# Performance work log

Hardware: AMD Instinct MI355X
Metric: run time of the kernel (lower is better)

The kernel has to match this reference:

```python
import jax, jax.numpy as jnp
import numpy as np

N_NODES = 50000
N_EDGES = 800000
D_IN = 128
D_HID = 128
GN_EPS = 1e-5
L2_EPS = 1e-12


def _gcn_conv(x, edge_index, W, b, num_nodes):
    """PyG GCNConv: symmetric normalization with self-loops; x [N, Fin]."""
    src, dst = edge_index[0], edge_index[1]
    loops = jnp.arange(num_nodes, dtype=src.dtype)
    src = jnp.concatenate([src, loops])
    dst = jnp.concatenate([dst, loops])
    ew = jnp.ones(src.shape[0], dtype=x.dtype)
    deg = jax.ops.segment_sum(ew, dst, num_segments=num_nodes)
    dinv = jnp.where(deg > 0, jax.lax.rsqrt(deg), 0.0)
    norm = dinv[src] * dinv[dst]                       # [E+N]
    xw = x @ W                                         # [N, Fout]
    msg = xw[src] * norm[:, None]                      # gather + scale
    out = jax.ops.segment_sum(msg, dst, num_segments=num_nodes)
    return out + b


def _message_norm(x, msg, scale):
    """PyG MessageNorm(learn_scale=True): x + scale * ||x|| * msg/||msg||."""
    msg_n = msg / jnp.maximum(jnp.linalg.norm(msg, axis=-1, keepdims=True), L2_EPS)
    x_norm = jnp.linalg.norm(x, axis=-1, keepdims=True)
    return x + scale * x_norm * msg_n


def _graph_norm(x, weight, bias, mean_scale):
    """PyG GraphNorm, single graph (batch all zeros)."""
    mean = jnp.mean(x, axis=0, keepdims=True)
    out = x - mean * mean_scale
    var = jnp.mean(out * out, axis=0, keepdims=True)
    return weight * out * jax.lax.rsqrt(var + GN_EPS) + bias


def _gelu(x):
    return jax.nn.gelu(x, approximate=False)


def setup_inputs() -> dict:
    key = jax.random.key(0)
    ks = jax.random.split(key, 4)
    X = jax.random.normal(ks[0], (D_IN, N_NODES), dtype=jnp.float32)
    edge_index = jax.random.randint(ks[1], (2, N_EDGES), 0, N_NODES, dtype=jnp.int64)
    W1 = jax.random.normal(ks[2], (D_IN, D_HID), dtype=jnp.float32) * (1.0 / np.sqrt(D_IN))
    b1 = jnp.zeros((D_HID,), dtype=jnp.float32)
    scale1 = jnp.ones((1,), dtype=jnp.float32)
    W2 = jax.random.normal(ks[3], (D_HID, D_IN), dtype=jnp.float32) * (1.0 / np.sqrt(D_HID))
    b2 = jnp.zeros((D_IN,), dtype=jnp.float32)
    scale2 = jnp.ones((1,), dtype=jnp.float32)
    gn_weight = jnp.ones((D_IN,), dtype=jnp.float32)
    gn_bias = jnp.zeros((D_IN,), dtype=jnp.float32)
    gn_mean_scale = jnp.ones((D_IN,), dtype=jnp.float32)
    return {"X": X, "edge_index": edge_index, "W1": W1, "b1": b1, "scale1": scale1,
            "W2": W2, "b2": b2, "scale2": scale2, "gn_weight": gn_weight,
            "gn_bias": gn_bias, "gn_mean_scale": gn_mean_scale}


def reference(X, edge_index, W1, b1, scale1, W2, b2, scale2,
              gn_weight, gn_bias, gn_mean_scale):
    x = X.T                                            # [N, D_IN]
    n = x.shape[0]
    # GCNChain 1
    f = _gelu(_message_norm(x, _gcn_conv(x, edge_index, W1, b1, n), scale1))
    # GCNChain 2
    f = _gelu(_message_norm(f, _gcn_conv(f, edge_index, W2, b2, n), scale2))
    # residual + GraphNorm + GELU
    return _gelu(_graph_norm(f + x, gn_weight, gn_bias, gn_mean_scale))
```

## Files before the change

### kernel.cpp

```cpp
#include <hip/hip_runtime.h>
#include <math.h>

#define D 128
#define CAP 64
#define NBUCK 98
#define BSZ   512
#define CAPB  10240

typedef _Float16 h8 __attribute__((ext_vector_type(8)));
typedef float f4x __attribute__((ext_vector_type(4)));

__device__ __forceinline__ float gelu_f(float v){
    return 0.5f * v * (1.0f + erff(v * 0.70710678f));
}

__global__ void k_init(float* colsum, float* colsq, int* gcur,
                       const float* __restrict__ W1, const float* __restrict__ W2,
                       _Float16* __restrict__ wz1, _Float16* __restrict__ wz2){
    int i = blockIdx.x*blockDim.x + threadIdx.x;
    if (i < D){ colsum[i] = 0.f; colsq[i] = 0.f; }
    if (i < NBUCK) gcur[i] = 0;
    if (i < 32768){
        const float* W = (i < 16384) ? W1 : W2;
        _Float16* wz   = (i < 16384) ? wz1 : wz2;
        int u = i & 16383;
        int jj = u & 7, l = (u>>3)&63, fi = u>>9;
        int kb = fi>>3, j = fi&7;
        int k = kb*32 + (l>>4)*8 + jj;
        int c = j*16 + (l&15);
        wz[u] = (_Float16)W[k*D + c];
    }
}

__global__ __launch_bounds__(256)
void k_part(const int* __restrict__ ei, int* __restrict__ gcur,
            unsigned int* __restrict__ ebin, int E){
    __shared__ int bcnt[NBUCK], bbase[NBUCK], bcur[NBUCK];
    int t = threadIdx.x;
    int chunk = (E + gridDim.x - 1) / gridDim.x;
    int e0 = blockIdx.x*chunk, e1 = min(e0 + chunk, E);
    if (t < NBUCK){ bcnt[t] = 0; bcur[t] = 0; }
    __syncthreads();
    int sl[13], dl[13];
    #pragma unroll
    for (int k = 0; k < 13; k++){
        int e = e0 + t + k*256;
        sl[k] = -1;
        if (e < e1){
            sl[k] = __builtin_nontemporal_load(&ei[e]);
            dl[k] = __builtin_nontemporal_load(&ei[E + e]);
            atomicAdd(&bcnt[dl[k] >> 9], 1);
        }
    }
    __syncthreads();
    if (t < NBUCK) bbase[t] = atomicAdd(&gcur[t], bcnt[t]);
    __syncthreads();
    #pragma unroll
    for (int k = 0; k < 13; k++){
        if (sl[k] >= 0){
            int d = dl[k], b = d >> 9;
            int p = atomicAdd(&bcur[b], 1);
            int idx = bbase[b] + p;
            if (idx < CAPB)
                ebin[(size_t)b*CAPB + idx] = ((unsigned)(d & (BSZ-1)) << 16) | (unsigned)sl[k];
        }
    }
}

__global__ __launch_bounds__(256)
void k_fill2(const unsigned int* __restrict__ ebin, const int* __restrict__ gcur,
             int* __restrict__ cnt, unsigned short* __restrict__ csrc, int N){
    __shared__ unsigned short slab[BSZ*CAP];
    __shared__ int lcnt[BSZ];
    int b = blockIdx.x, t = threadIdx.x;
    for (int i = t; i < BSZ; i += 256) lcnt[i] = 0;
    __syncthreads();
    int cntb = gcur[b]; if (cntb > CAPB) cntb = CAPB;
    const unsigned int* bp = ebin + (size_t)b*CAPB;
    for (int e = t; e < cntb; e += 256){
        unsigned pk = __builtin_nontemporal_load(&bp[e]);
        int dl = pk >> 16;
        int p = atomicAdd(&lcnt[dl], 1);
        if (p < CAP) slab[dl*CAP + p] = (unsigned short)(pk & 0xFFFF);
    }
    __syncthreads();
    int base = b*BSZ;
    int nvalid = N - base; if (nvalid > BSZ) nvalid = BSZ; if (nvalid < 0) nvalid = 0;
    uint4* dst = (uint4*)&csrc[(size_t)base*CAP];
    const uint4* src = (const uint4*)slab;
    for (int i = t; i < nvalid*8; i += 256) dst[i] = src[i];
    for (int i = t; i < nvalid; i += 256) cnt[base + i] = lcnt[i];
}

__launch_bounds__(256)
__global__ void k_gemm_mfma(const float* __restrict__ in, const h8* __restrict__ wz,
                            const int* __restrict__ cnt, _Float16* __restrict__ outh,
                            h8* __restrict__ xt16, int N){
    __shared__ _Float16 a_lds[8192];
    int t = threadIdx.x;
    int n0 = blockIdx.x * 64;

    #pragma unroll
    for (int i = 0; i < 32; i++){
        int idx = i*256 + t;
        int k = idx >> 6, nn = idx & 63;
        int n = n0 + nn;
        float v = (n < N) ? in[(size_t)k*N + n] : 0.f;
        int kb = k>>5, ks = k&31;
        int lane = (ks>>3)*16 + (nn&15);
        int w = nn>>4;
        a_lds[((kb*4 + w)*64 + lane)*8 + (ks&7)] = (_Float16)v;
    }
    __syncthreads();

    int w = t>>6, l = t&63;
    f4x acc[8];
    #pragma unroll
    for (int j = 0; j < 8; j++) acc[j] = (f4x){0.f, 0.f, 0.f, 0.f};
    #pragma unroll
    for (int kb = 0; kb < 4; kb++){
        h8 a = *(const h8*)&a_lds[((kb*4 + w)*64 + l)*8];
        #pragma unroll
        for (int j = 0; j < 8; j++){
            h8 b = wz[(kb*8 + j)*64 + l];
            acc[j] = __builtin_amdgcn_mfma_f32_16x16x32_f16(a, b, acc[j], 0, 0, 0);
        }
    }

    int quad = l>>4, m = l&15;
    #pragma unroll
    for (int r = 0; r < 4; r++){
        int node = n0 + w*16 + quad*4 + r;
        if (node < N){
            float dv = rsqrtf((float)(cnt[node] + 1));
            #pragma unroll
            for (int j = 0; j < 8; j++)
                outh[(size_t)node*D + j*16 + m] = (_Float16)(acc[j][r] * dv);
        }
    }

    {
        int node = t>>2, kb = t&3;
        int n = n0 + node;
        if (n < N){
            #pragma unroll
            for (int q = 0; q < 4; q++){
                h8 v = *(const h8*)&a_lds[((kb*4 + (node>>4))*64 + q*16 + (node&15))*8];
                xt16[(size_t)n*16 + kb*4 + q] = v;
            }
        }
    }
}

__launch_bounds__(256)
__global__ void k_gath1(const h8* __restrict__ y, const h8* __restrict__ resid,
                        const int* __restrict__ cnt,
                        const unsigned short* __restrict__ csrc,
                        const float* __restrict__ bias, const float* __restrict__ scale,
                        const h8* __restrict__ wz,
                        h8* __restrict__ f1out, _Float16* __restrict__ y2out, int N){
    __shared__ _Float16 a_lds[8192];
    int t = threadIdx.x;
    int n0 = blockIdx.x * 64;
    int g = t >> 4, lane = t & 15;
    int kb = lane >> 2, q = lane & 3;
    const float4* bp = (const float4*)&bias[lane*8];
    float4 b0 = bp[0], b1v = bp[1];
    float sc0 = scale[0];

    for (int it = 0; it < 4; it++){
        int n = n0 + it*16 + g;
        bool valid = (n < N);
        h8 a0 = {0,0,0,0,0,0,0,0}, a1 = a0, a2 = a0, a3 = a0;
        int m = 0; float dv = 1.f;
        if (valid){
            int mraw = cnt[n];
            dv = rsqrtf((float)(mraw + 1));
            m = (mraw < CAP) ? mraw : CAP;
            a0 = y[(size_t)n*16 + lane];
        }
        const unsigned short* sp = csrc + (size_t)n*CAP;
        int j = 0;
        for (; j + 8 <= m; j += 8){
            int s0 = sp[j+0], s1 = sp[j+1], s2 = sp[j+2], s3 = sp[j+3];
            int s4 = sp[j+4], s5 = sp[j+5], s6 = sp[j+6], s7 = sp[j+7];
            h8 v0 = y[(size_t)s0*16 + lane];
            h8 v1 = y[(size_t)s1*16 + lane];
            h8 v2 = y[(size_t)s2*16 + lane];
            h8 v3 = y[(size_t)s3*16 + lane];
            h8 v4 = y[(size_t)s4*16 + lane];
            h8 v5 = y[(size_t)s5*16 + lane];
            h8 v6 = y[(size_t)s6*16 + lane];
            h8 v7 = y[(size_t)s7*16 + lane];
            a0 += v0; a1 += v1; a2 += v2; a3 += v3;
            a0 += v4; a1 += v5; a2 += v6; a3 += v7;
        }
        for (; j + 4 <= m; j += 4){
            int s0 = sp[j+0], s1 = sp[j+1], s2 = sp[j+2], s3 = sp[j+3];
            h8 v0 = y[(size_t)s0*16 + lane];
            h8 v1 = y[(size_t)s1*16 + lane];
            h8 v2 = y[(size_t)s2*16 + lane];
            h8 v3 = y[(size_t)s3*16 + lane];
            a0 += v0; a1 += v1; a2 += v2; a3 += v3;
        }
        for (; j < m; j++) a1 += y[(size_t)sp[j]*16 + lane];
        h8 ah = (a0 + a1) + (a2 + a3);

        float c[8], r[8];
        float nc = 0.f, nr = 0.f;
        h8 rv = {0,0,0,0,0,0,0,0};
        if (valid) rv = resid[(size_t)n*16 + lane];
        #pragma unroll
        for (int i = 0; i < 8; i++){
            float bb = (i < 4) ? (&b0.x)[i] : (&b1v.x)[i-4];
            c[i] = bb + dv * (float)ah[i];
            nc += c[i]*c[i];
            r[i] = (float)rv[i];
            nr += r[i]*r[i];
        }
        #pragma unroll
        for (int mm = 8; mm > 0; mm >>= 1){
            nc += __shfl_xor(nc, mm, 64);
            nr += __shfl_xor(nr, mm, 64);
        }
        float scl = sc0 * sqrtf(nr) / fmaxf(sqrtf(nc), 1e-12f);
        h8 o;
        #pragma unroll
        for (int i = 0; i < 8; i++) o[i] = (_Float16)gelu_f(r[i] + scl*c[i]);
        if (valid) f1out[(size_t)n*16 + lane] = o;
        *(h8*)&a_lds[((kb*4 + it)*64 + q*16 + g)*8] = o;
    }
    __syncthreads();

    int w = t>>6, l = t&63;
    f4x acc[8];
    #pragma unroll
    for (int j = 0; j < 8; j++) acc[j] = (f4x){0.f, 0.f, 0.f, 0.f};
    #pragma unroll
    for (int kb2 = 0; kb2 < 4; kb2++){
        h8 a = *(const h8*)&a_lds[((kb2*4 + w)*64 + l)*8];
        #pragma unroll
        for (int j = 0; j < 8; j++){
            h8 b = wz[(kb2*8 + j)*64 + l];
            acc[j] = __builtin_amdgcn_mfma_f32_16x16x32_f16(a, b, acc[j], 0, 0, 0);
        }
    }
    int quad = l>>4, mcol = l&15;
    #pragma unroll
    for (int r2 = 0; r2 < 4; r2++){
        int node = n0 + w*16 + quad*4 + r2;
        if (node < N){
            float dv = rsqrtf((float)(cnt[node] + 1));
            #pragma unroll
            for (int j = 0; j < 8; j++)
                y2out[(size_t)node*D + j*16 + mcol] = (_Float16)(acc[j][r2] * dv);
        }
    }
}

__launch_bounds__(256)
__global__ void k_gather2(const h8* __restrict__ y, const h8* __restrict__ resid,
                          const h8* __restrict__ xorig,
                          const int* __restrict__ cnt,
                          const unsigned short* __restrict__ csrc,
                          const float* __restrict__ bias, const float* __restrict__ scale,
                          h8* __restrict__ out16, int N){
    int n = blockIdx.x*16 + (threadIdx.x >> 4);
    if (n >= N) return;
    int lane = threadIdx.x & 15;
    h8 a0 = y[(size_t)n*16 + lane];
    h8 a1 = {0,0,0,0,0,0,0,0}, a2 = a1, a3 = a1;
    int mraw = cnt[n];
    float dv = rsqrtf((float)(mraw + 1));
    int m = (mraw < CAP) ? mraw : CAP;
    const unsigned short* sp = csrc + (size_t)n*CAP;
    int j = 0;
    for (; j + 8 <= m; j += 8){
        int s0 = sp[j+0], s1 = sp[j+1], s2 = sp[j+2], s3 = sp[j+3];
        int s4 = sp[j+4], s5 = sp[j+5], s6 = sp[j+6], s7 = sp[j+7];
        h8 v0 = y[(size_t)s0*16 + lane];
        h8 v1 = y[(size_t)s1*16 + lane];
        h8 v2 = y[(size_t)s2*16 + lane];
        h8 v3 = y[(size_t)s3*16 + lane];
        h8 v4 = y[(size_t)s4*16 + lane];
        h8 v5 = y[(size_t)s5*16 + lane];
        h8 v6 = y[(size_t)s6*16 + lane];
        h8 v7 = y[(size_t)s7*16 + lane];
        a0 += v0; a1 += v1; a2 += v2; a3 += v3;
        a0 += v4; a1 += v5; a2 += v6; a3 += v7;
    }
    for (; j + 4 <= m; j += 4){
        int s0 = sp[j+0], s1 = sp[j+1], s2 = sp[j+2], s3 = sp[j+3];
        h8 v0 = y[(size_t)s0*16 + lane];
        h8 v1 = y[(size_t)s1*16 + lane];
        h8 v2 = y[(size_t)s2*16 + lane];
        h8 v3 = y[(size_t)s3*16 + lane];
        a0 += v0; a1 += v1; a2 += v2; a3 += v3;
    }
    for (; j < m; j++) a1 += y[(size_t)sp[j]*16 + lane];
    h8 ah = (a0 + a1) + (a2 + a3);

    const float4* bp = (const float4*)&bias[lane*8];
    float4 b0 = bp[0], b1v = bp[1];
    float c[8], r[8];
    float nc = 0.f, nr = 0.f;
    h8 rv = resid[(size_t)n*16 + lane];
    #pragma unroll
    for (int i = 0; i < 8; i++){
        float bb = (i < 4) ? (&b0.x)[i] : (&b1v.x)[i-4];
        c[i] = bb + dv * (float)ah[i];
        nc += c[i]*c[i];
        r[i] = (float)rv[i];
        nr += r[i]*r[i];
    }
    #pragma unroll
    for (int mm = 8; mm > 0; mm >>= 1){
        nc += __shfl_xor(nc, mm, 64);
        nr += __shfl_xor(nr, mm, 64);
    }
    float scl = scale[0] * sqrtf(nr) / fmaxf(sqrtf(nc), 1e-12f);
    h8 xv = xorig[(size_t)n*16 + lane];
    h8 o;
    #pragma unroll
    for (int i = 0; i < 8; i++)
        o[i] = (_Float16)(gelu_f(r[i] + scl*c[i]) + (float)xv[i]);
    out16[(size_t)n*16 + lane] = o;
}

__global__ void k_stats(const _Float16* __restrict__ h, float* colsum, float* colsq, int N){
    __shared__ float ls[256], ls2[256];
    int t = threadIdx.x;
    int f = t & 127, half = t >> 7;
    float s = 0.f, s2 = 0.f;
    for (int n = blockIdx.x*2 + half; n < N; n += gridDim.x*2){
        float v = (float)h[(size_t)n*D + f]; s += v; s2 += v*v;
    }
    ls[t] = s; ls2[t] = s2;
    __syncthreads();
    if (t < 128){
        s  = ls[t]  + ls[t+128];
        s2 = ls2[t] + ls2[t+128];
        atomicAdd(&colsum[f], s);
        atomicAdd(&colsq[f], s2);
    }
}

__global__ void k_final(const h8* __restrict__ h16,
                        const float* __restrict__ colsum, const float* __restrict__ colsq,
                        const float* __restrict__ gw, const float* __restrict__ gb,
                        const float* __restrict__ ms,
                        float* __restrict__ outp, int N){
    __shared__ float cf[D], sh[D];
    int t = threadIdx.x;
    if (t < D){
        float invN = 1.0f / (float)N;
        float mean = colsum[t] * invN;
        float c = mean * ms[t];
        float var = colsq[t]*invN - 2.f*c*mean + c*c;
        float a = gw[t] * rsqrtf(var + 1e-5f);
        cf[t] = a;
        sh[t] = gb[t] - c*a;
    }
    __syncthreads();
    int i = blockIdx.x*blockDim.x + t;
    if (i < N*16){
        int n = i >> 4, lane = i & 15;
        h8 v = h16[i];
        int f = lane*8;
        float4 o0, o1;
        o0.x = gelu_f((float)v[0]*cf[f+0] + sh[f+0]);
        o0.y = gelu_f((float)v[1]*cf[f+1] + sh[f+1]);
        o0.z = gelu_f((float)v[2]*cf[f+2] + sh[f+2]);
        o0.w = gelu_f((float)v[3]*cf[f+3] + sh[f+3]);
        o1.x = gelu_f((float)v[4]*cf[f+4] + sh[f+4]);
        o1.y = gelu_f((float)v[5]*cf[f+5] + sh[f+5]);
        o1.z = gelu_f((float)v[6]*cf[f+6] + sh[f+6]);
        o1.w = gelu_f((float)v[7]*cf[f+7] + sh[f+7]);
        *(float4*)&outp[(size_t)n*D + f]     = o0;
        *(float4*)&outp[(size_t)n*D + f + 4] = o1;
    }
}

extern "C" void kernel_launch(void* const* d_in, const int* in_sizes, int n_in,
                              void* d_out, int out_size, void* d_ws, size_t ws_size,
                              hipStream_t stream){
    const float* X   = (const float*)d_in[0];
    const int*   ei  = (const int*)  d_in[1];
    const float* W1  = (const float*)d_in[2];
    const float* b1  = (const float*)d_in[3];
    const float* s1  = (const float*)d_in[4];
    const float* W2  = (const float*)d_in[5];
    const float* b2  = (const float*)d_in[6];
    const float* s2  = (const float*)d_in[7];
    const float* gw  = (const float*)d_in[8];
    const float* gb  = (const float*)d_in[9];
    const float* gms = (const float*)d_in[10];
    int N = in_sizes[0] / D;
    int E = in_sizes[1] / 2;
    float* out = (float*)d_out;

    char* ws = (char*)d_ws;
    size_t o = 0;
    auto alloc = [&](size_t bytes)->void*{
        o = (o + 255) & ~(size_t)255;
        void* p = ws + o; o += bytes; return p;
    };
    int*            cnt    = (int*)           alloc((size_t)N * sizeof(int));
    unsigned short* csrc   = (unsigned short*)alloc((size_t)N * CAP * sizeof(unsigned short));
    unsigned int*   ebin   = (unsigned int*)  alloc((size_t)NBUCK * CAPB * sizeof(unsigned int));
    int*            gcur   = (int*)           alloc(NBUCK * sizeof(int));
    float*          colsum = (float*)         alloc(D * sizeof(float));
    float*          colsq  = (float*)         alloc(D * sizeof(float));
    _Float16*       wz1    = (_Float16*)      alloc(16384 * sizeof(_Float16));
    _Float16*       wz2    = (_Float16*)      alloc(16384 * sizeof(_Float16));
    _Float16*       A      = (_Float16*)      alloc((size_t)N * D * sizeof(_Float16));
    _Float16*       A2     = (_Float16*)      alloc((size_t)N * D * sizeof(_Float16));
    h8*             XT16   = (h8*)            alloc((size_t)N * D * sizeof(_Float16));
    h8*             F1     = (h8*)            alloc((size_t)N * D * sizeof(_Float16));
    h8*             B16    = (h8*)            alloc((size_t)N * D * sizeof(_Float16));

    k_init<<<128, 256, 0, stream>>>(colsum, colsq, gcur, W1, W2, wz1, wz2);
    k_part<<<256, 256, 0, stream>>>(ei, gcur, ebin, E);
    k_fill2<<<NBUCK, 256, 0, stream>>>(ebin, gcur, cnt, csrc, N);

    k_gemm_mfma<<<(N+63)/64, 256, 0, stream>>>(X, (const h8*)wz1, cnt, A, XT16, N);
    k_gath1<<<(N+63)/64, 256, 0, stream>>>((const h8*)A, XT16, cnt, csrc, b1, s1,
                                           (const h8*)wz2, F1, A2, N);
    k_gather2<<<(N+15)/16, 256, 0, stream>>>((const h8*)A2, F1, XT16,
                                             cnt, csrc, b2, s2, B16, N);
    k_stats<<<256, 256, 0, stream>>>((const _Float16*)B16, colsum, colsq, N);
    k_final<<<(N*16+255)/256, 256, 0, stream>>>(B16, colsum, colsq, gw, gb, gms, out, N);
}
```

Before: 263.9 us.

## Shrink gather1 blocks to 16 nodes and split MFMA output columns across warps

The first gather+GEMM kernel now handles 16 nodes per block instead of 64, so there is no serial 4-iteration gather loop and the grid has four times as many blocks. This gives more parallelism and latency hiding for the random neighbour gathers. The fused second-layer GEMM is re-split so each of the four waves computes two 16-column output tiles for the same 16 nodes, using a padded LDS layout that avoids bank conflicts. The cost is that each block reloads the weight matrix for only 16 nodes, so weight traffic per node rises fourfold.

```diff
diff --git a/kernel.cpp b/kernel.cpp
--- a/kernel.cpp
+++ b/kernel.cpp
@@ -159,101 +159,95 @@
                         const float* __restrict__ bias, const float* __restrict__ scale,
                         const h8* __restrict__ wz,
                         h8* __restrict__ f1out, _Float16* __restrict__ y2out, int N){
-    __shared__ _Float16 a_lds[8192];
+    __shared__ _Float16 a_lds[16*17*8];
     int t = threadIdx.x;
-    int n0 = blockIdx.x * 64;
+    int n0 = blockIdx.x * 16;
     int g = t >> 4, lane = t & 15;
-    int kb = lane >> 2, q = lane & 3;
+    int n = n0 + g;
+    bool valid = (n < N);
+
+    h8 a0 = {0,0,0,0,0,0,0,0}, a1 = a0, a2 = a0, a3 = a0;
+    int m = 0; float dv = 1.f;
+    if (valid){
+        int mraw = cnt[n];
+        dv = rsqrtf((float)(mraw + 1));
+        m = (mraw < CAP) ? mraw : CAP;
+        a0 = y[(size_t)n*16 + lane];
+    }
+    const unsigned short* sp = csrc + (size_t)n*CAP;
+    int j = 0;
+    for (; j + 8 <= m; j += 8){
+        int s0 = sp[j+0], s1 = sp[j+1], s2 = sp[j+2], s3 = sp[j+3];
+        int s4 = sp[j+4], s5 = sp[j+5], s6 = sp[j+6], s7 = sp[j+7];
+        h8 v0 = y[(size_t)s0*16 + lane];
+        h8 v1 = y[(size_t)s1*16 + lane];
+        h8 v2 = y[(size_t)s2*16 + lane];
+        h8 v3 = y[(size_t)s3*16 + lane];
+        h8 v4 = y[(size_t)s4*16 + lane];
+        h8 v5 = y[(size_t)s5*16 + lane];
+        h8 v6 = y[(size_t)s6*16 + lane];
+        h8 v7 = y[(size_t)s7*16 + lane];
+        a0 += v0; a1 += v1; a2 += v2; a3 += v3;
+        a0 += v4; a1 += v5; a2 += v6; a3 += v7;
+    }
+    for (; j + 4 <= m; j += 4){
+        int s0 = sp[j+0], s1 = sp[j+1], s2 = sp[j+2], s3 = sp[j+3];
+        h8 v0 = y[(size_t)s0*16 + lane];
+        h8 v1 = y[(size_t)s1*16 + lane];
+        h8 v2 = y[(size_t)s2*16 + lane];
+        h8 v3 = y[(size_t)s3*16 + lane];
+        a0 += v0; a1 += v1; a2 += v2; a3 += v3;
+    }
+    for (; j < m; j++) a1 += y[(size_t)sp[j]*16 + lane];
+    h8 ah = (a0 + a1) + (a2 + a3);
+
     const float4* bp = (const float4*)&bias[lane*8];
     float4 b0 = bp[0], b1v = bp[1];
-    float sc0 = scale[0];
-
-    for (int it = 0; it < 4; it++){
-        int n = n0 + it*16 + g;
-        bool valid = (n < N);
-        h8 a0 = {0,0,0,0,0,0,0,0}, a1 = a0, a2 = a0, a3 = a0;
-        int m = 0; float dv = 1.f;
-        if (valid){
-            int mraw = cnt[n];
-            dv = rsqrtf((float)(mraw + 1));
-            m = (mraw < CAP) ? mraw : CAP;
-            a0 = y[(size_t)n*16 + lane];
-        }
-        const unsigned short* sp = csrc + (size_t)n*CAP;
-        int j = 0;
-        for (; j + 8 <= m; j += 8){
-            int s0 = sp[j+0], s1 = sp[j+1], s2 = sp[j+2], s3 = sp[j+3];
-            int s4 = sp[j+4], s5 = sp[j+5], s6 = sp[j+6], s7 = sp[j+7];
-            h8 v0 = y[(size_t)s0*16 + lane];
-            h8 v1 = y[(size_t)s1*16 + lane];
-            h8 v2 = y[(size_t)s2*16 + lane];
-            h8 v3 = y[(size_t)s3*16 + lane];
-            h8 v4 = y[(size_t)s4*16 + lane];
-            h8 v5 = y[(size_t)s5*16 + lane];
-            h8 v6 = y[(size_t)s6*16 + lane];
-            h8 v7 = y[(size_t)s7*16 + lane];
-            a0 += v0; a1 += v1; a2 += v2; a3 += v3;
-            a0 += v4; a1 += v5; a2 += v6; a3 += v7;
-        }
-        for (; j + 4 <= m; j += 4){
-            int s0 = sp[j+0], s1 = sp[j+1], s2 = sp[j+2], s3 = sp[j+3];
-            h8 v0 = y[(size_t)s0*16 + lane];
-            h8 v1 = y[(size_t)s1*16 + lane];
-            h8 v2 = y[(size_t)s2*16 + lane];
-            h8 v3 = y[(size_t)s3*16 + lane];
-            a0 += v0; a1 += v1; a2 += v2; a3 += v3;
-        }
-        for (; j < m; j++) a1 += y[(size_t)sp[j]*16 + lane];
-        h8 ah = (a0 + a1) + (a2 + a3);
-
-        float c[8], r[8];
-        float nc = 0.f, nr = 0.f;
-        h8 rv = {0,0,0,0,0,0,0,0};
-        if (valid) rv = resid[(size_t)n*16 + lane];
-        #pragma unroll
-        for (int i = 0; i < 8; i++){
-            float bb = (i < 4) ? (&b0.x)[i] : (&b1v.x)[i-4];
-            c[i] = bb + dv * (float)ah[i];
-            nc += c[i]*c[i];
-            r[i] = (float)rv[i];
-            nr += r[i]*r[i];
-        }
-        #pragma unroll
-        for (int mm = 8; mm > 0; mm >>= 1){
-            nc += __shfl_xor(nc, mm, 64);
-            nr += __shfl_xor(nr, mm, 64);
-        }
-        float scl = sc0 * sqrtf(nr) / fmaxf(sqrtf(nc), 1e-12f);
-        h8 o;
+    float c[8], r[8];
+    float nc = 0.f, nr = 0.f;
+    h8 rv = {0,0,0,0,0,0,0,0};
+    if (valid) rv = resid[(size_t)n*16 + lane];
+    #pragma unroll
+    for (int i = 0; i < 8; i++){
+        float bb = (i < 4) ? (&b0.x)[i] : (&b1v.x)[i-4];
+        c[i] = bb + dv * (float)ah[i];
+        nc += c[i]*c[i];
+        r[i] = (float)rv[i];
+        nr += r[i]*r[i];
+    }
+    #pragma unroll
+    for (int mm = 8; mm > 0; mm >>= 1){
+        nc += __shfl_xor(nc, mm, 64);
+        nr += __shfl_xor(nr, mm, 64);
+    }
+    float scl = scale[0] * sqrtf(nr) / fmaxf(sqrtf(nc), 1e-12f);
+    h8 o = {0,0,0,0,0,0,0,0};
+    if (valid){
         #pragma unroll
         for (int i = 0; i < 8; i++) o[i] = (_Float16)gelu_f(r[i] + scl*c[i]);
-        if (valid) f1out[(size_t)n*16 + lane] = o;
-        *(h8*)&a_lds[((kb*4 + it)*64 + q*16 + g)*8] = o;
-    }
-    __syncthreads();
-
-    int w = t>>6, l = t&63;
-    f4x acc[8];
-    #pragma unroll
-    for (int j = 0; j < 8; j++) acc[j] = (f4x){0.f, 0.f, 0.f, 0.f};
-    #pragma unroll
-    for (int kb2 = 0; kb2 < 4; kb2++){
-        h8 a = *(const h8*)&a_lds[((kb2*4 + w)*64 + l)*8];
-        #pragma unroll
-        for (int j = 0; j < 8; j++){
-            h8 b = wz[(kb2*8 + j)*64 + l];
-            acc[j] = __builtin_amdgcn_mfma_f32_16x16x32_f16(a, b, acc[j], 0, 0, 0);
-        }
-    }
-    int quad = l>>4, mcol = l&15;
+        f1out[(size_t)n*16 + lane] = o;
+    }
+    *(h8*)&a_lds[(g*17 + lane)*8] = o;
+    __syncthreads();
+
+    int w = t >> 6, l = t & 63;
+    f4x acc0 = {0.f,0.f,0.f,0.f}, acc1 = acc0;
+    #pragma unroll
+    for (int kb = 0; kb < 4; kb++){
+        h8 a = *(const h8*)&a_lds[((l&15)*17 + kb*4 + (l>>4))*8];
+        h8 bb0 = wz[(kb*8 + w*2+0)*64 + l];
+        h8 bb1 = wz[(kb*8 + w*2+1)*64 + l];
+        acc0 = __builtin_amdgcn_mfma_f32_16x16x32_f16(a, bb0, acc0, 0, 0, 0);
+        acc1 = __builtin_amdgcn_mfma_f32_16x16x32_f16(a, bb1, acc1, 0, 0, 0);
+    }
+    int quad = l >> 4, mc = l & 15;
     #pragma unroll
     for (int r2 = 0; r2 < 4; r2++){
-        int node = n0 + w*16 + quad*4 + r2;
+        int node = n0 + quad*4 + r2;
         if (node < N){
-            float dv = rsqrtf((float)(cnt[node] + 1));
-            #pragma unroll
-            for (int j = 0; j < 8; j++)
-                y2out[(size_t)node*D + j*16 + mcol] = (_Float16)(acc[j][r2] * dv);
+            float dvn = rsqrtf((float)(cnt[node] + 1));
+            y2out[(size_t)node*D + (w*2+0)*16 + mc] = (_Float16)(acc0[r2] * dvn);
+            y2out[(size_t)node*D + (w*2+1)*16 + mc] = (_Float16)(acc1[r2] * dvn);
         }
     }
 }
@@ -424,7 +418,7 @@
     k_fill2<<<NBUCK, 256, 0, stream>>>(ebin, gcur, cnt, csrc, N);
 
     k_gemm_mfma<<<(N+63)/64, 256, 0, stream>>>(X, (const h8*)wz1, cnt, A, XT16, N);
-    k_gath1<<<(N+63)/64, 256, 0, stream>>>((const h8*)A, XT16, cnt, csrc, b1, s1,
+    k_gath1<<<(N+15)/16, 256, 0, stream>>>((const h8*)A, XT16, cnt, csrc, b1, s1,
                                            (const h8*)wz2, F1, A2, N);
     k_gather2<<<(N+15)/16, 256, 0, stream>>>((const h8*)A2, F1, XT16,
                                              cnt, csrc, b2, s2, B16, N);
```

Result: faster. 257.8 us (-2.3%).
